# Performance work log

Hardware: AMD Instinct MI355X
Metric: run time of the kernel (lower is better)

The kernel has to match this reference:

```python
import jax, jax.numpy as jnp
import numpy as np

N = 10000      # nodes
E = 160000     # edges
K = 32         # MC samples (dim 1 of inputs)
D_IN = 128
D_OUT = 32


def setup_inputs() -> dict:
    key = jax.random.key(0)
    k1, k2, k3, k4, k5 = jax.random.split(key, 5)
    x = jax.random.normal(k1, (N, K, D_IN), dtype=jnp.float32)
    # Glorot-uniform weight as in weight_variable_glorot
    init_range = np.sqrt(6.0 / (D_IN + D_OUT))
    weights = jax.random.uniform(k2, (D_IN, D_OUT), dtype=jnp.float32,
                                 minval=-init_range, maxval=init_range)
    edge_row = jax.random.randint(k3, (E,), 0, N, dtype=jnp.int32)
    edge_col = jax.random.randint(k4, (E,), 0, N, dtype=jnp.int32)
    edge_val = jax.random.uniform(k5, (E,), dtype=jnp.float32)
    return {"x": x, "weights": weights, "edge_row": edge_row,
            "edge_col": edge_col, "edge_val": edge_val}


def reference(x, weights, edge_row, edge_col, edge_val):
    # Original loops over K slices doing: dropout(p=0) -> x @ W -> spmm(adj, x) -> relu,
    # then concatenates along axis 1. Batched equivalent:
    h = jnp.einsum('nkd,de->nke', x, weights)            # [N, K, D_OUT]
    # sparse adj @ h : out[r] += val * h[c] for each edge (r, c, val)
    msg = h[edge_col] * edge_val[:, None, None]          # [E, K, D_OUT]
    agg = jax.ops.segment_sum(msg, edge_row, num_segments=N)  # [N, K, D_OUT]
    return jax.nn.relu(agg)
```

## Files before the change

kernel.cpp:

```cpp
#include <hip/hip_runtime.h>
#include <hip/hip_bf16.h>

#define KK 32
#define DIN 128
#define DOUT 32
#define NVEC (KK * DOUT)
#define NV4  (NVEC / 4)
#define MBKT 64
#define OCAP 4096

typedef float        vf4   __attribute__((ext_vector_type(4)));
typedef unsigned int vu4   __attribute__((ext_vector_type(4)));
typedef short        bf16x8 __attribute__((ext_vector_type(8)));

__device__ __forceinline__ float bfu2f(unsigned int u) {
    return __uint_as_float(u << 16);
}
__device__ __forceinline__ unsigned int f2bfu(float f) {
    __hip_bfloat16 b = __float2bfloat16(f);
    return *(unsigned short*)&b;
}

__global__ __launch_bounds__(256) void gemm_kernel(
    const float* __restrict__ x, const float* __restrict__ w,
    unsigned short* __restrict__ h)
{
    __shared__ float cbuf[4][16 * 33];
    const int tid  = threadIdx.x;
    const int lane = tid & 63;
    const int wid  = tid >> 6;
    const int q    = lane >> 4;
    const int lm   = lane & 15;

    bf16x8 bf[2][4];
    #pragma unroll
    for (int nt = 0; nt < 2; ++nt) {
        #pragma unroll
        for (int ks = 0; ks < 4; ++ks) {
            bf16x8 f;
            #pragma unroll
            for (int j = 0; j < 8; ++j) {
                int k = ks * 32 + q * 8 + j;
                f[j] = (short)f2bfu(w[k * DOUT + nt * 16 + lm]);
            }
            bf[nt][ks] = f;
        }
    }

    const int wgid = blockIdx.x * 4 + wid;
    float* cb = &cbuf[wid][0];

    #pragma unroll
    for (int it = 0; it < 2; ++it) {
        const int tile = wgid * 2 + it;
        const int r0   = tile * 16;
        const float* xrow = x + (size_t)(r0 + lm) * DIN + q * 8;

        vf4 acc0 = {0.f, 0.f, 0.f, 0.f};
        vf4 acc1 = {0.f, 0.f, 0.f, 0.f};

        #pragma unroll
        for (int ks = 0; ks < 4; ++ks) {
            vf4 a0 = *(const vf4*)(xrow + ks * 32);
            vf4 a1 = *(const vf4*)(xrow + ks * 32 + 4);
            bf16x8 af;
            af[0] = (short)f2bfu(a0.x); af[1] = (short)f2bfu(a0.y);
            af[2] = (short)f2bfu(a0.z); af[3] = (short)f2bfu(a0.w);
            af[4] = (short)f2bfu(a1.x); af[5] = (short)f2bfu(a1.y);
            af[6] = (short)f2bfu(a1.z); af[7] = (short)f2bfu(a1.w);
            acc0 = __builtin_amdgcn_mfma_f32_16x16x32_bf16(af, bf[0][ks], acc0, 0, 0, 0);
            acc1 = __builtin_amdgcn_mfma_f32_16x16x32_bf16(af, bf[1][ks], acc1, 0, 0, 0);
        }

        #pragma unroll
        for (int q2 = 0; q2 < 4; ++q2) {
            int row = q * 4 + q2;
            cb[row * 33 + lm]      = acc0[q2];
            cb[row * 33 + 16 + lm] = acc1[q2];
        }
        __syncthreads();

        const int rr = lane >> 2;
        const int cs = (lane & 3) * 8;
        const float* src = cb + rr * 33 + cs;
        vu4 packed;
        packed.x = f2bfu(src[0]) | (f2bfu(src[1]) << 16);
        packed.y = f2bfu(src[2]) | (f2bfu(src[3]) << 16);
        packed.z = f2bfu(src[4]) | (f2bfu(src[5]) << 16);
        packed.w = f2bfu(src[6]) | (f2bfu(src[7]) << 16);
        *(vu4*)(h + (size_t)(r0 + rr) * DOUT + cs) = packed;
        __syncthreads();
    }
}

__global__ void zero_kernel(int* __restrict__ p, int n) {
    int i = blockIdx.x * 256 + threadIdx.x;
    if (i < n) p[i] = 0;
}

__global__ void fill_bucket_kernel(
    const int* __restrict__ row, const int* __restrict__ col,
    const float* __restrict__ val, int* __restrict__ cursor,
    uint2* __restrict__ bedge,
    int* __restrict__ ocnt, int* __restrict__ orow,
    int* __restrict__ ocol, float* __restrict__ oval, int E)
{
    int i = blockIdx.x * 256 + threadIdx.x;
    if (i >= E) return;
    int r = row[i];
    int p = atomicAdd(&cursor[r], 1);
    if (p < MBKT) {
        uint2 e;
        e.x = (unsigned int)col[i];
        e.y = __float_as_uint(val[i]);
        bedge[r * MBKT + p] = e;
    } else {
        int q = atomicAdd(ocnt, 1);
        if (q < OCAP) {
            orow[q] = r;
            ocol[q] = col[i];
            oval[q] = val[i];
        }
    }
}

__global__ __launch_bounds__(256) void agg_kernel(
    const unsigned short* __restrict__ h, const int* __restrict__ cursor,
    const uint2* __restrict__ bedge,
    const int* __restrict__ ocnt, const int* __restrict__ orow,
    const int* __restrict__ ocol, const float* __restrict__ oval,
    float* __restrict__ out)
{
    const int tid  = threadIdx.x;
    const int half = tid >> 7;
    const int lt   = tid & 127;
    const int lane = tid & 63;
    const int r    = blockIdx.x * 2 + half;

    const int deg  = cursor[r];
    const int degb = deg < MBKT ? deg : MBKT;

    int   ec = 0;
    float ev = 0.f;
    if (lane < degb) {
        uint2 e = bedge[r * MBKT + lane];
        ec = (int)e.x;
        ev = __uint_as_float(e.y);
    }

    float acc[8];
    #pragma unroll
    for (int q = 0; q < 8; ++q) acc[q] = 0.f;

    #pragma unroll 4
    for (int j = 0; j < degb; ++j) {
        int   c = __shfl(ec, j, 64);
        float v = __shfl(ev, j, 64);
        vu4 p = *(const vu4*)(h + (size_t)c * NVEC + lt * 8);
        acc[0] += v * bfu2f(p.x & 0xffffu);
        acc[1] += v * bfu2f(p.x >> 16);
        acc[2] += v * bfu2f(p.y & 0xffffu);
        acc[3] += v * bfu2f(p.y >> 16);
        acc[4] += v * bfu2f(p.z & 0xffffu);
        acc[5] += v * bfu2f(p.z >> 16);
        acc[6] += v * bfu2f(p.w & 0xffffu);
        acc[7] += v * bfu2f(p.w >> 16);
    }

    int on = *ocnt;
    if (on > 0) {
        if (on > OCAP) on = OCAP;
        for (int q = 0; q < on; ++q) {
            if (orow[q] == r) {
                int   c = ocol[q];
                float v = oval[q];
                vu4 p = *(const vu4*)(h + (size_t)c * NVEC + lt * 8);
                acc[0] += v * bfu2f(p.x & 0xffffu);
                acc[1] += v * bfu2f(p.x >> 16);
                acc[2] += v * bfu2f(p.y & 0xffffu);
                acc[3] += v * bfu2f(p.y >> 16);
                acc[4] += v * bfu2f(p.z & 0xffffu);
                acc[5] += v * bfu2f(p.z >> 16);
                acc[6] += v * bfu2f(p.w & 0xffffu);
                acc[7] += v * bfu2f(p.w >> 16);
            }
        }
    }

    vf4 o0, o1;
    o0.x = fmaxf(acc[0], 0.f); o0.y = fmaxf(acc[1], 0.f);
    o0.z = fmaxf(acc[2], 0.f); o0.w = fmaxf(acc[3], 0.f);
    o1.x = fmaxf(acc[4], 0.f); o1.y = fmaxf(acc[5], 0.f);
    o1.z = fmaxf(acc[6], 0.f); o1.w = fmaxf(acc[7], 0.f);
    vf4* op = (vf4*)out + (size_t)r * NV4 + lt * 2;
    __builtin_nontemporal_store(o0, &op[0]);
    __builtin_nontemporal_store(o1, &op[1]);
}

extern "C" void kernel_launch(void* const* d_in, const int* in_sizes, int n_in,
                              void* d_out, int out_size, void* d_ws, size_t ws_size,
                              hipStream_t stream)
{
    const float* x    = (const float*)d_in[0];
    const float* w    = (const float*)d_in[1];
    const int*   erow = (const int*)d_in[2];
    const int*   ecol = (const int*)d_in[3];
    const float* eval = (const float*)d_in[4];
    float* out = (float*)d_out;

    const int E = in_sizes[2];
    const int N = in_sizes[0] / (KK * DIN);
    const int R = N * KK;

    char* ws = (char*)d_ws;
    size_t off = 0;
    auto take = [&](size_t bytes) {
        void* p = ws + off;
        off += (bytes + 15) & ~(size_t)15;
        return p;
    };
    unsigned short* h = (unsigned short*)take((size_t)R * DOUT * sizeof(unsigned short));
    int*   cursor = (int*)take((size_t)(N + 1) * sizeof(int));
    uint2* bedge  = (uint2*)take((size_t)N * MBKT * sizeof(uint2));
    int*   orow   = (int*)take((size_t)OCAP * sizeof(int));
    int*   ocol   = (int*)take((size_t)OCAP * sizeof(int));
    float* oval   = (float*)take((size_t)OCAP * sizeof(float));
    int*   ocnt   = cursor + N;
    (void)ws_size;

    gemm_kernel<<<R / 128, 256, 0, stream>>>(x, w, h);
    zero_kernel<<<(N + 1 + 255) / 256, 256, 0, stream>>>(cursor, N + 1);
    fill_bucket_kernel<<<(E + 255) / 256, 256, 0, stream>>>(
        erow, ecol, eval, cursor, bedge, ocnt, orow, ocol, oval, E);
    agg_kernel<<<N / 2, 256, 0, stream>>>(
        h, cursor, bedge, ocnt, orow, ocol, oval, out);
}
```

Measured before the change: 305.9 us.

## Fuse edge bucketing into GEMM launch and drop LDS transpose via interleaved h layout

Merges the edge bucket-fill kernel into the GEMM kernel as extra blocks, so the two independent stages share one launch and can overlap. The GEMM now stores MFMA accumulators directly as packed bf16 pairs in an interleaved column order, removing the shared-memory transpose and both barriers. The aggregation kernel's output store is remapped to undo the interleave. Each GEMM block now handles half as many tiles, so the per-block weight conversion is repeated more often.

After: 302.6 us. Within noise of the previous version (-1.1%).

```diff
diff --git a/kernel.cpp b/kernel.cpp
--- a/kernel.cpp
+++ b/kernel.cpp
@@ -5,12 +5,11 @@
 #define DIN 128
 #define DOUT 32
 #define NVEC (KK * DOUT)
-#define NV4  (NVEC / 4)
 #define MBKT 64
 #define OCAP 4096
 
-typedef float        vf4   __attribute__((ext_vector_type(4)));
-typedef unsigned int vu4   __attribute__((ext_vector_type(4)));
+typedef float        vf4    __attribute__((ext_vector_type(4)));
+typedef unsigned int vu4    __attribute__((ext_vector_type(4)));
 typedef short        bf16x8 __attribute__((ext_vector_type(8)));
 
 __device__ __forceinline__ float bfu2f(unsigned int u) {
@@ -21,12 +20,39 @@
     return *(unsigned short*)&b;
 }
 
-__global__ __launch_bounds__(256) void gemm_kernel(
+__global__ __launch_bounds__(256) void gemm_fill_kernel(
     const float* __restrict__ x, const float* __restrict__ w,
-    unsigned short* __restrict__ h)
+    unsigned short* __restrict__ h,
+    const int* __restrict__ erow, const int* __restrict__ ecol,
+    const float* __restrict__ eval, int* __restrict__ cursor,
+    uint2* __restrict__ bedge,
+    int* __restrict__ ocnt, int* __restrict__ orow,
+    int* __restrict__ ocol, float* __restrict__ oval,
+    int E, int FB)
 {
-    __shared__ float cbuf[4][16 * 33];
-    const int tid  = threadIdx.x;
+    const int tid = threadIdx.x;
+
+    if (blockIdx.x < (unsigned)FB) {
+        int i = blockIdx.x * 256 + tid;
+        if (i >= E) return;
+        int r = erow[i];
+        int p = atomicAdd(&cursor[r], 1);
+        if (p < MBKT) {
+            uint2 e;
+            e.x = (unsigned int)ecol[i];
+            e.y = __float_as_uint(eval[i]);
+            bedge[r * MBKT + p] = e;
+        } else {
+            int q = atomicAdd(ocnt, 1);
+            if (q < OCAP) {
+                orow[q] = r;
+                ocol[q] = ecol[i];
+                oval[q] = eval[i];
+            }
+        }
+        return;
+    }
+
     const int lane = tid & 63;
     const int wid  = tid >> 6;
     const int q    = lane >> 4;
@@ -47,81 +73,36 @@
         }
     }
 
-    const int wgid = blockIdx.x * 4 + wid;
-    float* cb = &cbuf[wid][0];
-
-    #pragma unroll
-    for (int it = 0; it < 2; ++it) {
-        const int tile = wgid * 2 + it;
-        const int r0   = tile * 16;
-        const float* xrow = x + (size_t)(r0 + lm) * DIN + q * 8;
-
-        vf4 acc0 = {0.f, 0.f, 0.f, 0.f};
-        vf4 acc1 = {0.f, 0.f, 0.f, 0.f};
-
-        #pragma unroll
-        for (int ks = 0; ks < 4; ++ks) {
-            vf4 a0 = *(const vf4*)(xrow + ks * 32);
-            vf4 a1 = *(const vf4*)(xrow + ks * 32 + 4);
-            bf16x8 af;
-            af[0] = (short)f2bfu(a0.x); af[1] = (short)f2bfu(a0.y);
-            af[2] = (short)f2bfu(a0.z); af[3] = (short)f2bfu(a0.w);
-            af[4] = (short)f2bfu(a1.x); af[5] = (short)f2bfu(a1.y);
-            af[6] = (short)f2bfu(a1.z); af[7] = (short)f2bfu(a1.w);
-            acc0 = __builtin_amdgcn_mfma_f32_16x16x32_bf16(af, bf[0][ks], acc0, 0, 0, 0);
-            acc1 = __builtin_amdgcn_mfma_f32_16x16x32_bf16(af, bf[1][ks], acc1, 0, 0, 0);
-        }
-
-        #pragma unroll
-        for (int q2 = 0; q2 < 4; ++q2) {
-            int row = q * 4 + q2;
-            cb[row * 33 + lm]      = acc0[q2];
-            cb[row * 33 + 16 + lm] = acc1[q2];
-        }
-        __syncthreads();
-
-        const int rr = lane >> 2;
-        const int cs = (lane & 3) * 8;
-        const float* src = cb + rr * 33 + cs;
-        vu4 packed;
-        packed.x = f2bfu(src[0]) | (f2bfu(src[1]) << 16);
-        packed.y = f2bfu(src[2]) | (f2bfu(src[3]) << 16);
-        packed.z = f2bfu(src[4]) | (f2bfu(src[5]) << 16);
-        packed.w = f2bfu(src[6]) | (f2bfu(src[7]) << 16);
-        *(vu4*)(h + (size_t)(r0 + rr) * DOUT + cs) = packed;
-        __syncthreads();
+    const int tile = (blockIdx.x - FB) * 4 + wid;
+    const int r0   = tile * 16;
+    const float* xrow = x + (size_t)(r0 + lm) * DIN + q * 8;
+
+    vf4 acc0 = {0.f, 0.f, 0.f, 0.f};
+    vf4 acc1 = {0.f, 0.f, 0.f, 0.f};
+
+    #pragma unroll
+    for (int ks = 0; ks < 4; ++ks) {
+        vf4 a0 = *(const vf4*)(xrow + ks * 32);
+        vf4 a1 = *(const vf4*)(xrow + ks * 32 + 4);
+        bf16x8 af;
+        af[0] = (short)f2bfu(a0.x); af[1] = (short)f2bfu(a0.y);
+        af[2] = (short)f2bfu(a0.z); af[3] = (short)f2bfu(a0.w);
+        af[4] = (short)f2bfu(a1.x); af[5] = (short)f2bfu(a1.y);
+        af[6] = (short)f2bfu(a1.z); af[7] = (short)f2bfu(a1.w);
+        acc0 = __builtin_amdgcn_mfma_f32_16x16x32_bf16(af, bf[0][ks], acc0, 0, 0, 0);
+        acc1 = __builtin_amdgcn_mfma_f32_16x16x32_bf16(af, bf[1][ks], acc1, 0, 0, 0);
+    }
+
+    #pragma unroll
+    for (int q2 = 0; q2 < 4; ++q2) {
+        unsigned int pk = f2bfu(acc0[q2]) | (f2bfu(acc1[q2]) << 16);
+        *(unsigned int*)(h + (size_t)(r0 + q * 4 + q2) * DOUT + lm * 2) = pk;
     }
 }
 
 __global__ void zero_kernel(int* __restrict__ p, int n) {
     int i = blockIdx.x * 256 + threadIdx.x;
     if (i < n) p[i] = 0;
-}
-
-__global__ void fill_bucket_kernel(
-    const int* __restrict__ row, const int* __restrict__ col,
-    const float* __restrict__ val, int* __restrict__ cursor,
-    uint2* __restrict__ bedge,
-    int* __restrict__ ocnt, int* __restrict__ orow,
-    int* __restrict__ ocol, float* __restrict__ oval, int E)
-{
-    int i = blockIdx.x * 256 + threadIdx.x;
-    if (i >= E) return;
-    int r = row[i];
-    int p = atomicAdd(&cursor[r], 1);
-    if (p < MBKT) {
-        uint2 e;
-        e.x = (unsigned int)col[i];
-        e.y = __float_as_uint(val[i]);
-        bedge[r * MBKT + p] = e;
-    } else {
-        int q = atomicAdd(ocnt, 1);
-        if (q < OCAP) {
-            orow[q] = r;
-            ocol[q] = col[i];
-            oval[q] = val[i];
-        }
-    }
 }
 
 __global__ __launch_bounds__(256) void agg_kernel(
@@ -139,6 +120,7 @@
 
     const int deg  = cursor[r];
     const int degb = deg < MBKT ? deg : MBKT;
+    const int on0  = *ocnt;
 
     int   ec = 0;
     float ev = 0.f;
@@ -167,9 +149,8 @@
         acc[7] += v * bfu2f(p.w >> 16);
     }
 
-    int on = *ocnt;
-    if (on > 0) {
-        if (on > OCAP) on = OCAP;
+    if (on0 > 0) {
+        int on = on0 > OCAP ? OCAP : on0;
         for (int q = 0; q < on; ++q) {
             if (orow[q] == r) {
                 int   c = ocol[q];
@@ -187,14 +168,14 @@
         }
     }
 
-    vf4 o0, o1;
-    o0.x = fmaxf(acc[0], 0.f); o0.y = fmaxf(acc[1], 0.f);
-    o0.z = fmaxf(acc[2], 0.f); o0.w = fmaxf(acc[3], 0.f);
-    o1.x = fmaxf(acc[4], 0.f); o1.y = fmaxf(acc[5], 0.f);
-    o1.z = fmaxf(acc[6], 0.f); o1.w = fmaxf(acc[7], 0.f);
-    vf4* op = (vf4*)out + (size_t)r * NV4 + lt * 2;
-    __builtin_nontemporal_store(o0, &op[0]);
-    __builtin_nontemporal_store(o1, &op[1]);
+    vf4 oA, oB;
+    oA.x = fmaxf(acc[0], 0.f); oA.y = fmaxf(acc[2], 0.f);
+    oA.z = fmaxf(acc[4], 0.f); oA.w = fmaxf(acc[6], 0.f);
+    oB.x = fmaxf(acc[1], 0.f); oB.y = fmaxf(acc[3], 0.f);
+    oB.z = fmaxf(acc[5], 0.f); oB.w = fmaxf(acc[7], 0.f);
+    float* obase = out + (size_t)r * NVEC + (lt >> 2) * 32 + (lt & 3) * 4;
+    __builtin_nontemporal_store(oA, (vf4*)obase);
+    __builtin_nontemporal_store(oB, (vf4*)(obase + 16));
 }
 
 extern "C" void kernel_launch(void* const* d_in, const int* in_sizes, int n_in,
@@ -228,10 +209,12 @@
     int*   ocnt   = cursor + N;
     (void)ws_size;
 
-    gemm_kernel<<<R / 128, 256, 0, stream>>>(x, w, h);
+    const int FB = (E + 255) / 256;
+    const int GB = (R / 16) / 4;
+
     zero_kernel<<<(N + 1 + 255) / 256, 256, 0, stream>>>(cursor, N + 1);
-    fill_bucket_kernel<<<(E + 255) / 256, 256, 0, stream>>>(
-        erow, ecol, eval, cursor, bedge, ocnt, orow, ocol, oval, E);
+    gemm_fill_kernel<<<FB + GB, 256, 0, stream>>>(
+        x, w, h, erow, ecol, eval, cursor, bedge, ocnt, orow, ocol, oval, E, FB);
     agg_kernel<<<N / 2, 256, 0, stream>>>(
         h, cursor, bedge, ocnt, orow, ocol, oval, out);
 }
```
